# Kernel tuning notes

Measured on AMD Instinct MI355X. Metric: run time of the kernel, lower is better.

The kernel has to match this reference:

```python
import jax, jax.numpy as jnp
import numpy as np

SW = 4096      # sliding_window
NH = 32        # n_heads
NKV = 8        # n_kv_heads
HD = 128       # head_dim
HIDDEN = 4096
B = 32         # batch (= max_batch_size)
GROUP = NH // NKV


def _nearest_32(n):
    return ((n + 31) // 32) * 32


def setup_inputs() -> dict:
    key = jax.random.key(0)
    ks = jax.random.split(key, 6)
    START = 5000  # start_pos > sliding_window -> wrapped-cache mask branch
    x = jax.random.normal(ks[0], (1, 1, B, HIDDEN), jnp.float32)
    wqkv = jax.random.normal(ks[1], (HIDDEN, (NH + 2 * NKV) * HD), jnp.float32) * 0.02
    wo = jax.random.normal(ks[2], (NH * HD, HIDDEN), jnp.float32) * 0.02
    cache_k = jax.random.normal(ks[3], (B, NKV, SW, HD), jnp.float32)
    cache_v = jax.random.normal(ks[4], (B, NKV, SW, HD), jnp.float32)
    # rotation matrix (freqs_to_rotation_matrix equivalent): block rotation for pos=START
    half = HD // 2
    inv_freq = 1.0 / (10000.0 ** (jnp.arange(half, dtype=jnp.float32) * 2.0 / HD))
    ang = START * inv_freq
    cos, sin = jnp.cos(ang), jnp.sin(ang)
    idx = jnp.arange(half)
    R = jnp.zeros((HD, HD), jnp.float32)
    R = R.at[idx, idx].set(cos).at[idx + half, idx + half].set(cos)
    R = R.at[idx, idx + half].set(sin).at[idx + half, idx].set(-sin)
    rot_mat = jnp.tile(R[None, None], (1, B, 1, 1))  # (1, B, HD, HD)
    # attention mask exactly as prepare_inputs builds it
    current = START % SW
    P = min(_nearest_32(START + 1), SW)
    NEG = jnp.finfo(jnp.float32).min
    mask = jnp.zeros((1, NH, B, P), jnp.float32)
    if START < SW:
        mask = mask.at[..., current + 1:].set(NEG)
    else:
        mask = mask.at[..., :current].set(NEG)
        mask = mask.at[..., SW - current:].set(NEG)
    return {"x": x, "rot_mat": rot_mat, "attn_mask": mask,
            "cache_k": cache_k, "cache_v": cache_v,
            "wqkv": wqkv, "wo": wo, "start_pos": START}


def reference(x, rot_mat, attn_mask, cache_k, cache_v, wqkv, wo, start_pos):
    P = min(_nearest_32(start_pos + 1), SW)    # padded_layer_past_len
    current = start_pos % SW                   # write slot in the ring cache
    # fused QKV projection: (1,1,B,H) @ (H,6144) -> take the (B,6144) slice
    xqkv = jnp.einsum('stbh,hf->stbf', x, wqkv)[0, 0]
    q = xqkv[:, :NH * HD].reshape(B, NH, HD)
    k = xqkv[:, NH * HD:(NH + NKV) * HD].reshape(B, NKV, HD)
    v = xqkv[:, (NH + NKV) * HD:].reshape(B, NKV, HD)
    # rotary via per-batch rotation matrix bmm
    R = rot_mat[0]                              # (B, HD, HD)
    q = jnp.einsum('bhd,bde->bhe', q, R)
    k = jnp.einsum('bkd,bde->bke', k, R)
    # update ring KV cache at slot `current`
    cache_k = cache_k.at[:, :, current, :].set(k)
    cache_v = cache_v.at[:, :, current, :].set(v)
    keys = cache_k[:, :, :P, :]                 # (B, NKV, P, HD)
    values = cache_v[:, :, :P, :]
    # grouped-query attention: q heads grouped per kv head
    qg = q.reshape(B, NKV, GROUP, HD)
    scores = jnp.einsum('bkgd,bkpd->bkgp', qg, keys) * (1.0 / np.sqrt(HD))
    # attn_mask is (1, NH, B, P); reorder to (B, NKV, GROUP, P)
    mask = jnp.transpose(attn_mask[0].reshape(NKV, GROUP, B, P), (2, 0, 1, 3))
    probs = jax.nn.softmax(scores + mask, axis=-1)
    out = jnp.einsum('bkgp,bkpd->bkgd', probs, values).reshape(B, NH * HD)
    dense = out @ wo                            # (B, HIDDEN)
    return dense.reshape(1, 1, B, HIDDEN)
```

## Files before the change

### kernel.cpp

```cpp
#include <hip/hip_runtime.h>
#include <hip/hip_bf16.h>
#include <stdint.h>

#define SW 4096
#define NH 32
#define NKV 8
#define GROUP 4
#define HD 128
#define HIDDEN 4096
#define BB 32
#define NQKV ((NH + 2*NKV)*HD)
#define CH 512
#define CHP (CH + 4)
#define NCH 8

template<int NW>
__global__ __launch_bounds__(256)
void gemm_f32(const float* __restrict__ A, const float* __restrict__ W,
              float* __restrict__ part, int kchunk) {
    const int n0 = blockIdx.x * 128;
    const int K0 = blockIdx.y * kchunk;
    const int t = threadIdx.x;
    const int tm = t >> 5;
    const int tn = t & 31;
    __shared__ float a_lds[32*36];
    __shared__ float w_lds[32*128];

    float acc[4][4];
    #pragma unroll
    for (int i = 0; i < 4; ++i)
        #pragma unroll
        for (int j = 0; j < 4; ++j) acc[i][j] = 0.f;

    for (int ks = 0; ks < kchunk; ks += 32) {
        {
            int m = t & 31, kl = t >> 5;
            #pragma unroll
            for (int i = 0; i < 4; ++i) {
                int k = kl + i*8;
                a_lds[k*36 + m] = A[(size_t)m*HIDDEN + K0 + ks + k];
            }
        }
        {
            #pragma unroll
            for (int i = 0; i < 4; ++i) {
                int j = t + i*256;
                int k = j >> 5, c = j & 31;
                const float4* src = (const float4*)(W + (size_t)(K0 + ks + k)*NW + n0);
                *(float4*)&w_lds[k*128 + c*4] = src[c];
            }
        }
        __syncthreads();
        #pragma unroll 8
        for (int k = 0; k < 32; ++k) {
            float4 a0 = *(const float4*)&a_lds[k*36 + tm*4];
            float4 w  = *(const float4*)&w_lds[k*128 + tn*4];
            float am[4] = {a0.x, a0.y, a0.z, a0.w};
            #pragma unroll
            for (int mi = 0; mi < 4; ++mi) {
                acc[mi][0] += am[mi]*w.x;
                acc[mi][1] += am[mi]*w.y;
                acc[mi][2] += am[mi]*w.z;
                acc[mi][3] += am[mi]*w.w;
            }
        }
        __syncthreads();
    }
    float* dst = part + (size_t)blockIdx.y*32*NW;
    #pragma unroll
    for (int mi = 0; mi < 4; ++mi) {
        int m = tm*4 + mi;
        float4 v = make_float4(acc[mi][0], acc[mi][1], acc[mi][2], acc[mi][3]);
        *(float4*)&dst[(size_t)m*NW + n0 + tn*4] = v;
    }
}

template<int NW>
__global__ __launch_bounds__(256)
void reduce_part(const float* __restrict__ part, float* __restrict__ out, int ksplit) {
    int idx = blockIdx.x*256 + threadIdx.x;
    if (idx >= 32*NW) return;
    float s = 0.f;
    for (int i = 0; i < ksplit; ++i) s += part[(size_t)i*32*NW + idx];
    out[idx] = s;
}

__global__ __launch_bounds__(256)
void rope_red(const float* __restrict__ part1, int KS, const float* __restrict__ rot,
              float* __restrict__ qrot, float* __restrict__ krot) {
    const int b = blockIdx.x;
    const int hbase = blockIdx.y * 8;
    const int t = threadIdx.x;
    __shared__ float Rl[64 * HD];
    __shared__ float qin[8 * HD];
    {
        const float* qsrc = part1 + (size_t)b * NQKV + (size_t)hbase * HD;
        float4 a = make_float4(0.f, 0.f, 0.f, 0.f);
        for (int i = 0; i < KS; ++i) {
            float4 v = ((const float4*)(qsrc + (size_t)i * 32 * NQKV))[t];
            a.x += v.x; a.y += v.y; a.z += v.z; a.w += v.w;
        }
        ((float4*)qin)[t] = a;
    }

    float acc[4] = {0.f, 0.f, 0.f, 0.f};
    for (int pass = 0; pass < 2; ++pass) {
        const float4* rsrc = (const float4*)(rot + (size_t)b * HD * HD + pass * 64 * HD);
        #pragma unroll
        for (int i = 0; i < 8; ++i) {
            int j = t + i * 256;
            ((float4*)Rl)[j] = rsrc[j];
        }
        __syncthreads();
        #pragma unroll
        for (int i = 0; i < 4; ++i) {
            int o = t + i * 256;
            int h = o >> 7, e = o & 127;
            float s = 0.f;
            for (int d = 0; d < 64; ++d) s += qin[h * HD + pass * 64 + d] * Rl[d * HD + e];
            acc[i] += s;
        }
        __syncthreads();
    }
    #pragma unroll
    for (int i = 0; i < 4; ++i) {
        int o = t + i * 256;
        int h = o >> 7, e = o & 127;
        int hh = hbase + h;
        if (hh < NH) qrot[((size_t)b * NH + hh) * HD + e] = acc[i];
        else         krot[((size_t)b * NKV + (hh - NH)) * HD + e] = acc[i];
    }
}

__device__ __forceinline__ void window_of(int sp, int& lo, int& hi, int& cur) {
    cur = ((sp % SW) + SW) % SW;
    if (sp < SW) { lo = 0; hi = sp + 1; } else { lo = cur; hi = SW - cur; }
}

__global__ __launch_bounds__(256)
void attn_chunk(const float* __restrict__ qrot, const float* __restrict__ krot,
                const float* __restrict__ part1, int KS,
                const float* __restrict__ ck, const float* __restrict__ cv,
                const int* __restrict__ spp, float* __restrict__ attnp) {
    const int bkv = blockIdx.x;
    const int b = bkv >> 3, kv = bkv & 7;
    const int c = blockIdx.y;
    const int t = threadIdx.x;
    int lo, hi, cur;
    window_of(spp[0], lo, hi, cur);
    const int n = hi - lo;
    const int base0 = c * CH;
    if (base0 >= n) return;
    const int nc = (n - base0 < CH) ? (n - base0) : CH;
    const size_t kvoff = (size_t)(b * NKV + kv) * SW * HD;
    const float scale = 0.08838834764831845f;

    __shared__ float q_lds[GROUP * HD];
    __shared__ float scl[GROUP * CHP];
    __shared__ float vnew[HD];
    __shared__ float mg[GROUP], lg[GROUP];
    __shared__ float pp[4][GROUP][HD];

    {
        const size_t qoff = ((size_t)b * NH + kv * GROUP) * HD;
        q_lds[t]       = qrot[qoff + t];
        q_lds[256 + t] = qrot[qoff + 256 + t];
    }
    if (t < HD) {
        const float* vsrc = part1 + (size_t)b * NQKV + (size_t)(NH + NKV) * HD + kv * HD + t;
        float s = 0.f;
        for (int i = 0; i < KS; ++i) s += vsrc[(size_t)i * 32 * NQKV];
        vnew[t] = s;
    }
    __syncthreads();

    {
        const int dsl  = t & 7;
        const int posw = (t >> 3) & 7;
        const int w    = t >> 6;
        float4 qreg[GROUP][4];
        #pragma unroll
        for (int g = 0; g < GROUP; ++g)
            #pragma unroll
            for (int j = 0; j < 4; ++j)
                qreg[g][j] = *(const float4*)&q_lds[g*HD + j*32 + dsl*4];

        const float* krow = krot + ((size_t)b * NKV + kv) * HD;
        #pragma unroll 1
        for (int it = 0; it < CH/32; ++it) {
            const int r = it*32 + w*8 + posw;
            const bool valid = (r < nc);
            float s0 = 0.f, s1 = 0.f, s2 = 0.f, s3 = 0.f;
            if (valid) {
                const int p = lo + base0 + r;
                const float* kbase = (p == cur) ? krow : (ck + kvoff + (size_t)p * HD);
                #pragma unroll
                for (int j = 0; j < 4; ++j) {
                    float4 kk = *(const float4*)&kbase[j*32 + dsl*4];
                    s0 += kk.x*qreg[0][j].x + kk.y*qreg[0][j].y + kk.z*qreg[0][j].z + kk.w*qreg[0][j].w;
                    s1 += kk.x*qreg[1][j].x + kk.y*qreg[1][j].y + kk.z*qreg[1][j].z + kk.w*qreg[1][j].w;
                    s2 += kk.x*qreg[2][j].x + kk.y*qreg[2][j].y + kk.z*qreg[2][j].z + kk.w*qreg[2][j].w;
                    s3 += kk.x*qreg[3][j].x + kk.y*qreg[3][j].y + kk.z*qreg[3][j].z + kk.w*qreg[3][j].w;
                }
            }
            s0 += __shfl_xor(s0, 1); s0 += __shfl_xor(s0, 2); s0 += __shfl_xor(s0, 4);
            s1 += __shfl_xor(s1, 1); s1 += __shfl_xor(s1, 2); s1 += __shfl_xor(s1, 4);
            s2 += __shfl_xor(s2, 1); s2 += __shfl_xor(s2, 2); s2 += __shfl_xor(s2, 4);
            s3 += __shfl_xor(s3, 1); s3 += __shfl_xor(s3, 2); s3 += __shfl_xor(s3, 4);
            float sg = (dsl == 0) ? s0 : (dsl == 1) ? s1 : (dsl == 2) ? s2 : s3;
            if (dsl < GROUP)
                scl[dsl * CHP + r] = valid ? sg * scale : -3.0e38f;
        }
    }
    __syncthreads();

    {
        const int w = t >> 6, l = t & 63;
        float v[8];
        float m = -3.0e38f;
        #pragma unroll
        for (int j = 0; j < 8; ++j) {
            v[j] = scl[w*CHP + l + 64*j];
            m = fmaxf(m, v[j]);
        }
        #pragma unroll
        for (int off = 32; off; off >>= 1) m = fmaxf(m, __shfl_xor(m, off));
        float ss = 0.f;
        #pragma unroll
        for (int j = 0; j < 8; ++j) {
            float e = __expf(v[j] - m);
            scl[w*CHP + l + 64*j] = e;
            ss += e;
        }
        #pragma unroll
        for (int off = 32; off; off >>= 1) ss += __shfl_xor(ss, off);
        if (l == 0) { mg[w] = m; lg[w] = ss; }
    }
    __syncthreads();

    {
        const int d2 = (t & 63) * 2, rg = t >> 6;
        const int r0 = rg * (CH/4);
        const float2 vn2 = *(const float2*)&vnew[d2];
        float a0[GROUP], a1[GROUP];
        #pragma unroll
        for (int g = 0; g < GROUP; ++g) { a0[g] = 0.f; a1[g] = 0.f; }
        #pragma unroll 1
        for (int i = 0; i < CH/16; ++i) {
            const int r = r0 + i*4;
            float4 pr[GROUP];
            #pragma unroll
            for (int g = 0; g < GROUP; ++g)
                pr[g] = *(const float4*)&scl[g*CHP + r];
            #pragma unroll
            for (int k = 0; k < 4; ++k) {
                const int rr = r + k;
                const int p = lo + base0 + rr;
                float2 v;
                if (rr >= nc)      v = make_float2(0.f, 0.f);
                else if (p == cur) v = vn2;
                else               v = *(const float2*)&cv[kvoff + (size_t)p * HD + d2];
                const float p0 = (k == 0) ? pr[0].x : (k == 1) ? pr[0].y : (k == 2) ? pr[0].z : pr[0].w;
                const float p1 = (k == 0) ? pr[1].x : (k == 1) ? pr[1].y : (k == 2) ? pr[1].z : pr[1].w;
                const float p2 = (k == 0) ? pr[2].x : (k == 1) ? pr[2].y : (k == 2) ? pr[2].z : pr[2].w;
                const float p3 = (k == 0) ? pr[3].x : (k == 1) ? pr[3].y : (k == 2) ? pr[3].z : pr[3].w;
                a0[0] += p0 * v.x; a1[0] += p0 * v.y;
                a0[1] += p1 * v.x; a1[1] += p1 * v.y;
                a0[2] += p2 * v.x; a1[2] += p2 * v.y;
                a0[3] += p3 * v.x; a1[3] += p3 * v.y;
            }
        }
        #pragma unroll
        for (int g = 0; g < GROUP; ++g) {
            pp[rg][g][d2]     = a0[g];
            pp[rg][g][d2 + 1] = a1[g];
        }
    }
    __syncthreads();
    {
        float* op = attnp + ((size_t)bkv * NCH + c) * 520;
        #pragma unroll
        for (int j = 0; j < 2; ++j) {
            int v = t + 256*j;
            int g = v >> 7, d = v & 127;
            op[g * HD + d] = pp[0][g][d] + pp[1][g][d] + pp[2][g][d] + pp[3][g][d];
        }
        if (t < GROUP) {
            op[512 + t] = mg[t];
            op[516 + t] = lg[t];
        }
    }
}

__global__ __launch_bounds__(512)
void attn_reduce(const float* __restrict__ attnp, const int* __restrict__ spp,
                 float* __restrict__ aout) {
    const int bkv = blockIdx.x;
    const int b = bkv >> 3, kv = bkv & 7;
    const int g = threadIdx.x >> 7, d = threadIdx.x & 127;
    int lo, hi, cur;
    window_of(spp[0], lo, hi, cur);
    const int n = hi - lo;
    const int nch = (n + CH - 1) / CH;
    float M = -3.0e38f;
    for (int c = 0; c < nch; ++c)
        M = fmaxf(M, attnp[((size_t)bkv * NCH + c) * 520 + 512 + g]);
    float L = 0.f, O = 0.f;
    for (int c = 0; c < nch; ++c) {
        const float* op = attnp + ((size_t)bkv * NCH + c) * 520;
        float w = __expf(op[512 + g] - M);
        L += w * op[516 + g];
        O += w * op[g * HD + d];
    }
    aout[(size_t)b * NH * HD + (size_t)(kv * GROUP + g) * HD + d] = O / L;
}

__global__ __launch_bounds__(512)
void attn_kernel(const float* __restrict__ qrot, const float* __restrict__ krot,
                 const float* __restrict__ qkv,
                 const float* __restrict__ ck, const float* __restrict__ cv,
                 const int* __restrict__ spp, float* __restrict__ aout) {
    const int b = blockIdx.x >> 3, kv = blockIdx.x & 7;
    const int t = threadIdx.x;
    int lo, hi, cur;
    window_of(spp[0], lo, hi, cur);
    const int n = hi - lo;
    const size_t kvoff = (size_t)(b * NKV + kv) * SW * HD;
    const float scale = 0.08838834764831845f;

    __shared__ float sc[GROUP * 2304];
    __shared__ float q_lds[GROUP * HD];
    __shared__ float redb[512];
    __shared__ float ssum_s[GROUP];

    q_lds[t] = qrot[((size_t)b * NH + kv * GROUP) * HD + t];
    __syncthreads();

    for (int i = t; i < n; i += 512) {
        int p = lo + i;
        float s[GROUP] = {0.f, 0.f, 0.f, 0.f};
        if (p == cur) {
            const float* kr = krot + ((size_t)b * NKV + kv) * HD;
            for (int d = 0; d < HD; ++d) {
                float kd = kr[d];
                #pragma unroll
                for (int g = 0; g < GROUP; ++g) s[g] += kd * q_lds[g * HD + d];
            }
        } else {
            const float* kp = ck + kvoff + (size_t)p * HD;
            for (int c = 0; c < 32; ++c) {
                float4 kk = ((const float4*)kp)[c];
                #pragma unroll
                for (int g = 0; g < GROUP; ++g)
                    s[g] += kk.x * q_lds[g * HD + c * 4] + kk.y * q_lds[g * HD + c * 4 + 1]
                          + kk.z * q_lds[g * HD + c * 4 + 2] + kk.w * q_lds[g * HD + c * 4 + 3];
            }
        }
        #pragma unroll
        for (int g = 0; g < GROUP; ++g)
            sc[g * 2304 + i] = s[g] * scale;
    }
    __syncthreads();

    for (int g = 0; g < GROUP; ++g) {
        float m = -3.0e38f;
        for (int i = t; i < n; i += 512) m = fmaxf(m, sc[g * 2304 + i]);
        redb[t] = m;
        __syncthreads();
        for (int w = 256; w > 0; w >>= 1) {
            if (t < w) redb[t] = fmaxf(redb[t], redb[t + w]);
            __syncthreads();
        }
        float mx = redb[0];
        __syncthreads();
        float s = 0.f;
        for (int i = t; i < n; i += 512) {
            float e = __expf(sc[g * 2304 + i] - mx);
            sc[g * 2304 + i] = e;
            s += e;
        }
        redb[t] = s;
        __syncthreads();
        for (int w = 256; w > 0; w >>= 1) {
            if (t < w) redb[t] += redb[t + w];
            __syncthreads();
        }
        if (t == 0) ssum_s[g] = redb[0];
        __syncthreads();
    }

    {
        const int g = t >> 7, d = t & 127;
        const float vn = qkv[(size_t)b * NQKV + (size_t)(NH + NKV) * HD + kv * HD + d];
        float acc = 0.f;
        for (int r = 0; r < n; ++r) {
            int p = lo + r;
            float v = (p == cur) ? vn : cv[kvoff + (size_t)p * HD + d];
            acc += sc[g * 2304 + r] * v;
        }
        aout[(size_t)b * NH * HD + (size_t)(kv * GROUP + g) * HD + d] = acc / ssum_s[g];
    }
}

extern "C" void kernel_launch(void* const* d_in, const int* in_sizes, int n_in,
                              void* d_out, int out_size, void* d_ws, size_t ws_size,
                              hipStream_t stream) {
    (void)out_size;
    static const long long CS[8] = {131072LL, 524288LL, 4194304LL, 134217728LL,
                                    134217728LL, 25165824LL, 16777216LL, 1LL};
    const void* Pp[8];
    bool canonical = (n_in == 8);
    if (canonical)
        for (int i = 0; i < 8; ++i)
            if ((long long)in_sizes[i] != CS[i]) { canonical = false; break; }
    if (canonical) {
        for (int i = 0; i < 8; ++i) Pp[i] = d_in[i];
    } else {
        bool used[64] = {false};
        for (int j = 0; j < 8; ++j) {
            Pp[j] = d_in[0];
            for (int i = 0; i < n_in && i < 64; ++i)
                if (!used[i] && (long long)in_sizes[i] == CS[j]) { used[i] = true; Pp[j] = d_in[i]; break; }
        }
    }

    const float* x    = (const float*)Pp[0];
    const float* rot  = (const float*)Pp[1];
    const float* ck   = (const float*)Pp[3];
    const float* cv   = (const float*)Pp[4];
    const float* wqkv = (const float*)Pp[5];
    const float* wo   = (const float*)Pp[6];
    const int*   sp   = (const int*)Pp[7];

    float* qkv  = (float*)d_ws;
    float* qrot = qkv  + (size_t)BB*NQKV;
    float* krot = qrot + (size_t)BB*NH*HD;
    float* aout = krot + (size_t)BB*NKV*HD;
    float* attnp= aout + (size_t)BB*NH*HD;
    float* part1= attnp + (size_t)BB*NKV*NCH*520;

    const size_t head_bytes = ((size_t)BB*(NQKV + NH*HD + NKV*HD + NH*HD)
                               + (size_t)BB*NKV*NCH*520) * 4;
    const size_t p1_bytes   = (size_t)32*32*NQKV*4;
    const size_t p2_bytes   = (size_t)32*32*HIDDEN*4;

    if (ws_size >= head_bytes + p1_bytes + p2_bytes) {
        const int KS1 = 32, KS2 = 32;
        float* part2 = part1 + (size_t)KS1*32*NQKV;

        gemm_f32<NQKV><<<dim3(NQKV/128, KS1), 256, 0, stream>>>(x, wqkv, part1, HIDDEN/KS1);
        rope_red<<<dim3(BB, 5), 256, 0, stream>>>(part1, KS1, rot, qrot, krot);
        attn_chunk<<<dim3(BB*NKV, NCH), 256, 0, stream>>>(qrot, krot, part1, KS1, ck, cv, sp, attnp);
        attn_reduce<<<BB*NKV, 512, 0, stream>>>(attnp, sp, aout);
        gemm_f32<HIDDEN><<<dim3(HIDDEN/128, KS2), 256, 0, stream>>>(aout, wo, part2, HIDDEN/KS2);
        reduce_part<HIDDEN><<<(BB*HIDDEN + 255)/256, 256, 0, stream>>>(part2, (float*)d_out, KS2);
    } else {
        size_t per_ks = (size_t)32*(NQKV + HIDDEN) * 4;
        size_t avail = (ws_size > head_bytes) ? ws_size - head_bytes : 0;
        int KS = 1;
        if      (avail >= 8*per_ks) KS = 8;
        else if (avail >= 4*per_ks) KS = 4;
        else if (avail >= 2*per_ks) KS = 2;
        float* part2 = part1 + (size_t)KS*32*NQKV;

        gemm_f32<NQKV><<<dim3(NQKV/128, KS), 256, 0, stream>>>(x, wqkv, part1, HIDDEN/KS);
        reduce_part<NQKV><<<(BB*NQKV + 255)/256, 256, 0, stream>>>(part1, qkv, KS);
        rope_red<<<dim3(BB, 5), 256, 0, stream>>>(part1, KS, rot, qrot, krot);
        attn_kernel<<<BB*NKV, 512, 0, stream>>>(qrot, krot, qkv, ck, cv, sp, aout);
        gemm_f32<HIDDEN><<<dim3(HIDDEN/128, KS), 256, 0, stream>>>(aout, wo, part2, HIDDEN/KS);
        reduce_part<HIDDEN><<<(BB*HIDDEN + 255)/256, 256, 0, stream>>>(part2, (float*)d_out, KS);
    }
}
```

Baseline: 236.9 us.

## Fuse split-K and chunk reductions into producer kernels via last-block atomic counters

The separate attn_reduce and reduce_part launches are removed. Each producer block now increments an atomic counter after writing its partials, and the last block to arrive does the combine. Counters are zeroed inside rope_red. This cuts two kernel launches and their tail gaps, at the cost of a serialized reduction tail done by a few blocks, plus extra fences and atomics.

```diff
diff --git a/kernel.cpp b/kernel.cpp
--- a/kernel.cpp
+++ b/kernel.cpp
@@ -77,6 +77,86 @@
 
 template<int NW>
 __global__ __launch_bounds__(256)
+void gemm_f32_red(const float* __restrict__ A, const float* __restrict__ W,
+                  float* __restrict__ part, float* __restrict__ out,
+                  int* __restrict__ cnt, int kchunk, int ksplit) {
+    const int n0 = blockIdx.x * 128;
+    const int K0 = blockIdx.y * kchunk;
+    const int t = threadIdx.x;
+    const int tm = t >> 5;
+    const int tn = t & 31;
+    __shared__ float a_lds[32*36];
+    __shared__ float w_lds[32*128];
+    __shared__ int winner_s;
+
+    float acc[4][4];
+    #pragma unroll
+    for (int i = 0; i < 4; ++i)
+        #pragma unroll
+        for (int j = 0; j < 4; ++j) acc[i][j] = 0.f;
+
+    for (int ks = 0; ks < kchunk; ks += 32) {
+        {
+            int m = t & 31, kl = t >> 5;
+            #pragma unroll
+            for (int i = 0; i < 4; ++i) {
+                int k = kl + i*8;
+                a_lds[k*36 + m] = A[(size_t)m*HIDDEN + K0 + ks + k];
+            }
+        }
+        {
+            #pragma unroll
+            for (int i = 0; i < 4; ++i) {
+                int j = t + i*256;
+                int k = j >> 5, c = j & 31;
+                const float4* src = (const float4*)(W + (size_t)(K0 + ks + k)*NW + n0);
+                *(float4*)&w_lds[k*128 + c*4] = src[c];
+            }
+        }
+        __syncthreads();
+        #pragma unroll 8
+        for (int k = 0; k < 32; ++k) {
+            float4 a0 = *(const float4*)&a_lds[k*36 + tm*4];
+            float4 w  = *(const float4*)&w_lds[k*128 + tn*4];
+            float am[4] = {a0.x, a0.y, a0.z, a0.w};
+            #pragma unroll
+            for (int mi = 0; mi < 4; ++mi) {
+                acc[mi][0] += am[mi]*w.x;
+                acc[mi][1] += am[mi]*w.y;
+                acc[mi][2] += am[mi]*w.z;
+                acc[mi][3] += am[mi]*w.w;
+            }
+        }
+        __syncthreads();
+    }
+    float* dst = part + (size_t)blockIdx.y*32*NW;
+    #pragma unroll
+    for (int mi = 0; mi < 4; ++mi) {
+        int m = tm*4 + mi;
+        float4 v = make_float4(acc[mi][0], acc[mi][1], acc[mi][2], acc[mi][3]);
+        *(float4*)&dst[(size_t)m*NW + n0 + tn*4] = v;
+    }
+
+    __threadfence();
+    __syncthreads();
+    if (t == 0) winner_s = atomicAdd(&cnt[blockIdx.x], 1);
+    __syncthreads();
+    if (winner_s == ksplit - 1) {
+        __threadfence();
+        #pragma unroll
+        for (int i = 0; i < 16; ++i) {
+            int e = t + i*256;
+            int m = e >> 7, col = e & 127;
+            size_t off = (size_t)m*NW + n0 + col;
+            float s = 0.f;
+            for (int sl = 0; sl < ksplit; ++sl) s += part[(size_t)sl*32*NW + off];
+            out[off] = s;
+        }
+    }
+}
+
+template<int NW>
+__global__ __launch_bounds__(256)
 void reduce_part(const float* __restrict__ part, float* __restrict__ out, int ksplit) {
     int idx = blockIdx.x*256 + threadIdx.x;
     if (idx >= 32*NW) return;
@@ -87,10 +167,14 @@
 
 __global__ __launch_bounds__(256)
 void rope_red(const float* __restrict__ part1, int KS, const float* __restrict__ rot,
-              float* __restrict__ qrot, float* __restrict__ krot) {
+              float* __restrict__ qrot, float* __restrict__ krot,
+              int* __restrict__ cnt, int ncnt) {
     const int b = blockIdx.x;
     const int hbase = blockIdx.y * 8;
     const int t = threadIdx.x;
+    if (b == 0 && blockIdx.y == 0) {
+        for (int i = t; i < ncnt; i += 256) cnt[i] = 0;
+    }
     __shared__ float Rl[64 * HD];
     __shared__ float qin[8 * HD];
     {
@@ -141,7 +225,8 @@
 void attn_chunk(const float* __restrict__ qrot, const float* __restrict__ krot,
                 const float* __restrict__ part1, int KS,
                 const float* __restrict__ ck, const float* __restrict__ cv,
-                const int* __restrict__ spp, float* __restrict__ attnp) {
+                const int* __restrict__ spp, float* __restrict__ attnp,
+                int* __restrict__ cnt, float* __restrict__ aout) {
     const int bkv = blockIdx.x;
     const int b = bkv >> 3, kv = bkv & 7;
     const int c = blockIdx.y;
@@ -152,6 +237,7 @@
     const int base0 = c * CH;
     if (base0 >= n) return;
     const int nc = (n - base0 < CH) ? (n - base0) : CH;
+    const int nch = (n + CH - 1) / CH;
     const size_t kvoff = (size_t)(b * NKV + kv) * SW * HD;
     const float scale = 0.08838834764831845f;
 
@@ -160,6 +246,7 @@
     __shared__ float vnew[HD];
     __shared__ float mg[GROUP], lg[GROUP];
     __shared__ float pp[4][GROUP][HD];
+    __shared__ int winner_s;
 
     {
         const size_t qoff = ((size_t)b * NH + kv * GROUP) * HD;
@@ -288,6 +375,30 @@
         if (t < GROUP) {
             op[512 + t] = mg[t];
             op[516 + t] = lg[t];
+        }
+    }
+
+    __threadfence();
+    __syncthreads();
+    if (t == 0) winner_s = atomicAdd(&cnt[bkv], 1);
+    __syncthreads();
+    if (winner_s == nch - 1) {
+        __threadfence();
+        #pragma unroll
+        for (int j = 0; j < 2; ++j) {
+            int v = t + 256*j;
+            int g = v >> 7, d = v & 127;
+            float M = -3.0e38f;
+            for (int cc = 0; cc < nch; ++cc)
+                M = fmaxf(M, attnp[((size_t)bkv * NCH + cc) * 520 + 512 + g]);
+            float L = 0.f, O = 0.f;
+            for (int cc = 0; cc < nch; ++cc) {
+                const float* opc = attnp + ((size_t)bkv * NCH + cc) * 520;
+                float w = __expf(opc[512 + g] - M);
+                L += w * opc[516 + g];
+                O += w * opc[g * HD + d];
+            }
+            aout[(size_t)b * NH * HD + (size_t)(kv * GROUP + g) * HD + d] = O / L;
         }
     }
 }
@@ -443,17 +554,21 @@
                                + (size_t)BB*NKV*NCH*520) * 4;
     const size_t p1_bytes   = (size_t)32*32*NQKV*4;
     const size_t p2_bytes   = (size_t)32*32*HIDDEN*4;
-
-    if (ws_size >= head_bytes + p1_bytes + p2_bytes) {
+    const size_t cnt_bytes  = 4096;
+
+    if (ws_size >= head_bytes + p1_bytes + p2_bytes + cnt_bytes) {
         const int KS1 = 32, KS2 = 32;
         float* part2 = part1 + (size_t)KS1*32*NQKV;
+        int* cnt = (int*)(part2 + (size_t)KS2*32*HIDDEN);
+        const int NCNT = 288;
 
         gemm_f32<NQKV><<<dim3(NQKV/128, KS1), 256, 0, stream>>>(x, wqkv, part1, HIDDEN/KS1);
-        rope_red<<<dim3(BB, 5), 256, 0, stream>>>(part1, KS1, rot, qrot, krot);
-        attn_chunk<<<dim3(BB*NKV, NCH), 256, 0, stream>>>(qrot, krot, part1, KS1, ck, cv, sp, attnp);
-        attn_reduce<<<BB*NKV, 512, 0, stream>>>(attnp, sp, aout);
-        gemm_f32<HIDDEN><<<dim3(HIDDEN/128, KS2), 256, 0, stream>>>(aout, wo, part2, HIDDEN/KS2);
-        reduce_part<HIDDEN><<<(BB*HIDDEN + 255)/256, 256, 0, stream>>>(part2, (float*)d_out, KS2);
+        rope_red<<<dim3(BB, 5), 256, 0, stream>>>(part1, KS1, rot, qrot, krot, cnt, NCNT);
+        attn_chunk<<<dim3(BB*NKV, NCH), 256, 0, stream>>>(qrot, krot, part1, KS1, ck, cv, sp,
+                                                          attnp, cnt, aout);
+        gemm_f32_red<HIDDEN><<<dim3(HIDDEN/128, KS2), 256, 0, stream>>>(aout, wo, part2,
+                                                                        (float*)d_out, cnt + 256,
+                                                                        HIDDEN/KS2, KS2);
     } else {
         size_t per_ks = (size_t)32*(NQKV + HIDDEN) * 4;
         size_t avail = (ws_size > head_bytes) ? ws_size - head_bytes : 0;
@@ -462,10 +577,11 @@
         else if (avail >= 4*per_ks) KS = 4;
         else if (avail >= 2*per_ks) KS = 2;
         float* part2 = part1 + (size_t)KS*32*NQKV;
+        int* cnt = (int*)(part2 + (size_t)KS*32*HIDDEN);
 
         gemm_f32<NQKV><<<dim3(NQKV/128, KS), 256, 0, stream>>>(x, wqkv, part1, HIDDEN/KS);
         reduce_part<NQKV><<<(BB*NQKV + 255)/256, 256, 0, stream>>>(part1, qkv, KS);
-        rope_red<<<dim3(BB, 5), 256, 0, stream>>>(part1, KS, rot, qrot, krot);
+        rope_red<<<dim3(BB, 5), 256, 0, stream>>>(part1, KS, rot, qrot, krot, cnt, 0);
         attn_kernel<<<BB*NKV, 512, 0, stream>>>(qrot, krot, qkv, ck, cv, sp, aout);
         gemm_f32<HIDDEN><<<dim3(HIDDEN/128, KS), 256, 0, stream>>>(aout, wo, part2, HIDDEN/KS);
         reduce_part<HIDDEN><<<(BB*HIDDEN + 255)/256, 256, 0, stream>>>(part2, (float*)d_out, KS);
```

Result: slower. 655.0 us (+176.5%).
